# Optimization experiments

Measured on AMD Instinct MI355X. Metric: run time of the kernel, lower is better.

## Reference

```python
import jax, jax.numpy as jnp
import numpy as np

B, D_IN, LAT, C = 16384, 512, 64, 8
HID = [1024, 512, 256]

def _lin(k, fi, fo, scale=0.02):
    k1, k2 = jax.random.split(k)
    return jax.random.normal(k1, (fi, fo), jnp.float32) * scale, jax.random.normal(k2, (fo,), jnp.float32) * scale

def _lin_c(k, fi, fo, scale=0.02):
    k1, k2 = jax.random.split(k)
    return jax.random.normal(k1, (C, fi, fo), jnp.float32) * scale, jax.random.normal(k2, (C, fo), jnp.float32) * scale

def setup_inputs() -> dict:
    key = jax.random.key(0)
    ks = jax.random.split(key, 16)
    x = jax.random.normal(ks[0], (B, D_IN), jnp.float32)
    cluster_labels = jax.random.randint(ks[1], (B,), 0, C, jnp.int32)
    eps = jax.random.normal(ks[2], (B, LAT), jnp.float32)
    # encoder: shared(512->1024), unshared(1024->512), shared(512->256)
    enc_W0, enc_b0 = _lin(ks[3], D_IN, HID[0])
    enc_Wu, enc_bu = _lin_c(ks[4], HID[0], HID[1])
    enc_W2, enc_b2 = _lin(ks[5], HID[1], HID[2])
    # shared latent heads
    mu_W, mu_b = _lin(ks[6], HID[2], LAT)
    lv_W, lv_b = _lin(ks[7], HID[2], LAT)
    # decoder (hidden_dims reversed = [256,512,1024]): unshared(64->256), shared(256->512), unshared(512->1024)
    dec_Wu0, dec_bu0 = _lin_c(ks[8], LAT, HID[2])
    dec_W1, dec_b1 = _lin(ks[9], HID[2], HID[1])
    dec_Wu2, dec_bu2 = _lin_c(ks[10], HID[1], HID[0])
    # per-cluster final layer (1024 -> input_dim), no activation (all-continuous)
    fin_W, fin_b = _lin_c(ks[11], HID[0], D_IN)
    return dict(x=x, cluster_labels=cluster_labels, eps=eps,
                enc_W0=enc_W0, enc_b0=enc_b0, enc_Wu=enc_Wu, enc_bu=enc_bu,
                enc_W2=enc_W2, enc_b2=enc_b2, mu_W=mu_W, mu_b=mu_b,
                lv_W=lv_W, lv_b=lv_b, dec_Wu0=dec_Wu0, dec_bu0=dec_bu0,
                dec_W1=dec_W1, dec_b1=dec_b1, dec_Wu2=dec_Wu2, dec_bu2=dec_bu2,
                fin_W=fin_W, fin_b=fin_b)

def _unshared(h, W, b, labels):
    # per-cluster GEMM then row-wise combine (mask-based dispatch, no row reorder)
    y = jnp.einsum('bi,cio->bco', h, W) + b[None]  # [B, C, out]
    return jnp.take_along_axis(y, labels[:, None, None], axis=1)[:, 0, :]

def reference(x, cluster_labels, eps,
              enc_W0, enc_b0, enc_Wu, enc_bu, enc_W2, enc_b2,
              mu_W, mu_b, lv_W, lv_b,
              dec_Wu0, dec_bu0, dec_W1, dec_b1, dec_Wu2, dec_bu2,
              fin_W, fin_b):
    lbl = cluster_labels.astype(jnp.int32)
    # encoder
    h = jax.nn.relu(x @ enc_W0 + enc_b0)
    h = jax.nn.relu(_unshared(h, enc_Wu, enc_bu, lbl))
    h = jax.nn.relu(h @ enc_W2 + enc_b2)
    mu = h @ mu_W + mu_b
    logvar = h @ lv_W + lv_b
    # reparameterize
    z = mu + jnp.exp(0.5 * logvar) * eps
    # decoder
    h = jax.nn.relu(_unshared(z, dec_Wu0, dec_bu0, lbl))
    h = jax.nn.relu(h @ dec_W1 + dec_b1)
    h = jax.nn.relu(_unshared(h, dec_Wu2, dec_bu2, lbl))
    # per-cluster final output layer (identity activation: all-continuous)
    recon = _unshared(h, fin_W, fin_b, lbl)
    return recon
```

## Files before the change

kernel.cpp:

```cpp
#include <hip/hip_runtime.h>

typedef _Float16 f16;
typedef __attribute__((ext_vector_type(8))) _Float16 f16x8;
typedef __attribute__((ext_vector_type(4))) _Float16 f16x4;
typedef __attribute__((ext_vector_type(4))) float    f32x4;

#define B_ROWS 16384
#define MPAD   17408
#define MTILES 136
#define NBLK   64

typedef __attribute__((address_space(1))) void as1_void;
typedef __attribute__((address_space(3))) void as3_void;

__device__ __forceinline__ void gl_lds16(const void* g, void* l) {
    __builtin_amdgcn_global_load_lds((const as1_void*)g, (as3_void*)l, 16, 0, 0);
}


__global__ __launch_bounds__(256) void k_prep(const int* __restrict__ lbl, int* __restrict__ blockhist,
                                              int* __restrict__ rowmap,
                                              const float* __restrict__ mb_, const float* __restrict__ lb_,
                                              float* __restrict__ bz, f16* __restrict__ zerob) {
    int b = blockIdx.x, t = threadIdx.x;
    int i = b * 256 + t;
    rowmap[i] = -1;
    if (b < NBLK) {
        __shared__ int h[8];
        if (t < 8) h[t] = 0;
        __syncthreads();
        atomicAdd(&h[lbl[i]], 1);
        __syncthreads();
        if (t < 8) blockhist[b * 8 + t] = h[t];
    } else if (b == NBLK) {
        if (t < 64) zerob[t] = (f16)0.f;
        if (t < 64) bz[t] = mb_[t];
        else if (t < 128) bz[t] = lb_[t - 64];
    }
}

__global__ void k_offsets(const int* __restrict__ blockhist, int* offs, int* tilec, int* blockbase) {
    __shared__ int tot[8];
    __shared__ int so[9];
    int t = threadIdx.x;
    if (t < 8) {
        int s = 0;
        for (int b = 0; b < NBLK; ++b) s += blockhist[b * 8 + t];
        tot[t] = s;
    }
    __syncthreads();
    if (t == 0) {
        int o = 0;
        for (int c = 0; c < 8; ++c) { so[c] = o; o += (tot[c] + 127) & ~127; }
        so[8] = o;
        for (int c = 0; c < 9; ++c) offs[c] = so[c];
    }
    __syncthreads();
    if (t < 8) {
        int run = so[t];
        for (int b = 0; b < NBLK; ++b) {
            blockbase[b * 8 + t] = run;
            run += blockhist[b * 8 + t];
        }
    }
    if (t < MTILES) {
        int row = t * 128, c = 7;
        for (int cc = 0; cc < 8; ++cc)
            if (row >= so[cc] && row < so[cc + 1]) c = cc;
        tilec[t] = c;
    }
}

__global__ __launch_bounds__(256) void k_scatter(const int* __restrict__ lbl,
                                                 const int* __restrict__ blockbase,
                                                 int* __restrict__ rowmap) {
    __shared__ int cur[8];
    if (threadIdx.x < 8) cur[threadIdx.x] = blockbase[blockIdx.x * 8 + threadIdx.x];
    __syncthreads();
    int i = blockIdx.x * 256 + threadIdx.x;
    int c = lbl[i];
    int pos = atomicAdd(&cur[c], 1);
    rowmap[pos] = i;
}


struct Seg { const float* s; f16* d; int K, N, b0, nx, ny; long sCS, dCS; };
struct SegTab { Seg g[10]; };

__global__ __launch_bounds__(256) void k_trans(SegTab tab, const float* __restrict__ x, f16* __restrict__ xh) {
    int bid = blockIdx.x;
    int t = threadIdx.x;
    if (bid < tab.g[1].b0) {
        size_t i = (size_t)bid * 256 + t;
        float4 a = ((const float4*)x)[2 * i];
        float4 b = ((const float4*)x)[2 * i + 1];
        f16x8 o = {(f16)a.x, (f16)a.y, (f16)a.z, (f16)a.w,
                   (f16)b.x, (f16)b.y, (f16)b.z, (f16)b.w};
        ((f16x8*)xh)[i] = o;
        return;
    }
    int s = 9;
    while (bid < tab.g[s].b0) --s;
    Seg sg = tab.g[s];
    int lb = bid - sg.b0;
    int nxy = sg.nx * sg.ny;
    int z = lb / nxy; int r = lb - z * nxy;
    int by = r / sg.nx; int bx = r - by * sg.nx;
    const float* src = sg.s + (size_t)z * sg.sCS;
    f16* dst = sg.d + (size_t)z * sg.dCS;
    int n0 = bx * 64, k0 = by * 64;
    __shared__ float ld[64][64];
    int cr = t >> 4, cc = (t & 15) * 4;
    #pragma unroll
    for (int i = 0; i < 4; ++i) {
        float4 v = *(const float4*)(src + (size_t)(k0 + cr + 16 * i) * sg.N + n0 + cc);
        *(float4*)&ld[cr + 16 * i][cc] = v;
    }
    __syncthreads();
    int n = t & 63, gp = t >> 6;
    #pragma unroll
    for (int p = 0; p < 2; ++p) {
        int g = gp + 4 * p;
        f16x8 o;
        #pragma unroll
        for (int j = 0; j < 8; ++j) o[j] = (f16)ld[g * 8 + j][n];
        *(f16x8*)(dst + (size_t)(n0 + n) * sg.K + k0 + g * 8) = o;
    }
}


template<int GATHER, int PERW, int RELU, int EPI>
__global__ __launch_bounds__(256) void gemm_k(
    const f16* __restrict__ A, const f16* __restrict__ Wt,
    const float* __restrict__ bias, f16* __restrict__ Out, float* __restrict__ OutF,
    const float* __restrict__ eps,
    const int* __restrict__ rowmap, const int* __restrict__ tilec,
    const f16* __restrict__ zerobuf, int K, int N)
{
    __shared__ __align__(16) char smem[32768];
    const int tid  = threadIdx.x;
    const int wave = tid >> 6;
    const int lane = tid & 63;

    const int id  = blockIdx.x;
    const int xcd = id & 7;
    const int jj  = id >> 3;
    const int tm  = (jj % 17) * 8 + xcd;
    const int tn  = jj / 17;
    const int r0 = tm * 128, n0 = tn * 128;

    const f16* wb = Wt;
    const float* bb = bias;
    if (PERW) {
        int c = tilec[tm];
        wb += (size_t)c * K * N;
        bb += (size_t)c * N;
    }

    const int srow = tid >> 2;
    const int sg   = tid & 3;
    const int xk16 = (sg ^ ((srow >> 1) & 3)) * 16;
    const size_t rowB = (size_t)K * 2;

    const char* pa[2]; size_t stepA[2];
    #pragma unroll
    for (int p = 0; p < 2; ++p) {
        int gr = r0 + p * 64 + srow;
        if (GATHER) {
            int g = rowmap[gr];
            if (g >= 0) { pa[p] = (const char*)(A + (size_t)g * K) + xk16; stepA[p] = 64; }
            else        { pa[p] = (const char*)zerobuf;                    stepA[p] = 0;  }
        } else {
            pa[p] = (const char*)(A + (size_t)gr * K) + xk16; stepA[p] = 64;
        }
    }
    const char* pb = (const char*)(wb + (size_t)(n0 + srow) * K) + xk16;
    const size_t pbOff = 64 * rowB;

    const int mb = (wave >> 1) * 64;
    const int nb = (wave & 1) * 64;
    const int quad = lane >> 4;
    const int r16  = lane & 15;
    const int off  = (quad ^ ((r16 >> 1) & 3)) * 16;

    float bv[4];
    #pragma unroll
    for (int j = 0; j < 4; ++j) bv[j] = bb[n0 + nb + j * 16 + r16];

    f32x4 acc[4][4];
    #pragma unroll
    for (int i = 0; i < 4; ++i)
        #pragma unroll
        for (int j = 0; j < 4; ++j)
            acc[i][j] = (f32x4){0.f, 0.f, 0.f, 0.f};

    auto stage = [&](char* dst) {
        gl_lds16(pa[0], dst        + wave * 1024);
        gl_lds16(pa[1], dst + 4096 + wave * 1024);
        gl_lds16(pb,           dst + 8192  + wave * 1024);
        gl_lds16(pb + pbOff,   dst + 12288 + wave * 1024);
        pa[0] += stepA[0]; pa[1] += stepA[1];
        pb += 64;
    };

    auto compute = [&](const char* base) {
        const char* lA = base;
        const char* lB = base + 8192;
        f16x8 af[4], bf[4];
        #pragma unroll
        for (int i = 0; i < 4; ++i)
            af[i] = *(const f16x8*)(lA + (mb + i * 16 + r16) * 64 + off);
        #pragma unroll
        for (int j = 0; j < 4; ++j)
            bf[j] = *(const f16x8*)(lB + (nb + j * 16 + r16) * 64 + off);
        #pragma unroll
        for (int i = 0; i < 4; ++i)
            #pragma unroll
            for (int j = 0; j < 4; ++j)
                acc[i][j] = __builtin_amdgcn_mfma_f32_16x16x32_f16(af[i], bf[j], acc[i][j], 0, 0, 0);
    };

    const int nk = K >> 5;
    stage(smem);
    __syncthreads();
    int cur = 0;
    for (int kb = 0; kb < nk - 1; ++kb) {
        stage(smem + ((cur ^ 1) << 14));
        compute(smem + (cur << 14));
        __syncthreads();
        cur ^= 1;
    }
    compute(smem + (cur << 14));

    if (EPI == 2) {
        __syncthreads();
        #pragma unroll
        for (int i = 0; i < 4; ++i) {
            #pragma unroll
            for (int r = 0; r < 4; ++r) {
                int lr = mb + i * 16 + quad * 4 + r;
                #pragma unroll
                for (int j = 0; j < 4; ++j) {
                    int lc = nb + j * 16 + r16;
                    float v = acc[i][j][r] + bv[j];
                    *(f16*)(smem + lr * 256 + ((((lc >> 3) ^ (lr & 7))) << 4) + ((lc & 7) << 1)) = (f16)v;
                }
            }
        }
        __syncthreads();
        const int col = tid & 63;
        const int rb  = tid >> 6;
        for (int rr = 0; rr < 32; ++rr) {
            int row = rb * 32 + rr;
            int g = rowmap[r0 + row];
            float e = (g >= 0) ? eps[(size_t)g * 64 + col] : 0.f;
            float mu = (float)*(const f16*)(smem + row * 256 + ((((col >> 3) ^ (row & 7))) << 4) + ((col & 7) << 1));
            int c2 = col + 64;
            float lv = (float)*(const f16*)(smem + row * 256 + ((((c2 >> 3) ^ (row & 7))) << 4) + ((c2 & 7) << 1));
            Out[(size_t)(r0 + row) * 64 + col] = (f16)(mu + expf(0.5f * lv) * e);
        }
        return;
    }

    #pragma unroll
    for (int i = 0; i < 4; ++i) {
        #pragma unroll
        for (int r = 0; r < 4; ++r) {
            int orow = r0 + mb + i * 16 + quad * 4 + r;
            int g = 0;
            if (EPI == 1) g = rowmap[orow];
            #pragma unroll
            for (int j = 0; j < 4; ++j) {
                int ocol = n0 + nb + j * 16 + r16;
                float v = acc[i][j][r] + bv[j];
                if (RELU) v = fmaxf(v, 0.f);
                if (EPI == 1) {
                    if (g >= 0) OutF[(size_t)g * N + ocol] = v;
                } else {
                    Out[(size_t)orow * N + ocol] = (f16)v;
                }
            }
        }
    }
}


extern "C" void kernel_launch(void* const* d_in, const int* in_sizes, int n_in,
                              void* d_out, int out_size, void* d_ws, size_t ws_size,
                              hipStream_t stream) {
    const float* x      = (const float*)d_in[0];
    const int*   lbl    = (const int*)  d_in[1];
    const float* eps    = (const float*)d_in[2];
    const float* enc_W0 = (const float*)d_in[3];
    const float* enc_b0 = (const float*)d_in[4];
    const float* enc_Wu = (const float*)d_in[5];
    const float* enc_bu = (const float*)d_in[6];
    const float* enc_W2 = (const float*)d_in[7];
    const float* enc_b2 = (const float*)d_in[8];
    const float* mu_W   = (const float*)d_in[9];
    const float* mu_b   = (const float*)d_in[10];
    const float* lv_W   = (const float*)d_in[11];
    const float* lv_b   = (const float*)d_in[12];
    const float* dWu0   = (const float*)d_in[13];
    const float* dbu0   = (const float*)d_in[14];
    const float* dW1    = (const float*)d_in[15];
    const float* db1    = (const float*)d_in[16];
    const float* dWu2   = (const float*)d_in[17];
    const float* dbu2   = (const float*)d_in[18];
    const float* finW   = (const float*)d_in[19];
    const float* finb   = (const float*)d_in[20];
    float* out = (float*)d_out;
    (void)in_sizes; (void)n_in; (void)out_size; (void)ws_size;

    char* base = (char*)d_ws;
    size_t off = 0;
    auto alloc = [&](size_t bytes) { char* r = base + off; off = (off + bytes + 255) & ~(size_t)255; return r; };
    f16* xh     = (f16*)alloc((size_t)B_ROWS * 512 * 2);
    f16* buf1   = (f16*)alloc((size_t)MPAD * 1024 * 2);
    f16* buf2   = (f16*)alloc((size_t)MPAD * 512 * 2);
    f16* buf3   = (f16*)alloc((size_t)MPAD * 256 * 2);
    f16* zb     = (f16*)alloc((size_t)MPAD * 64 * 2);
    f16* w0t    = (f16*)alloc(1024ul * 512 * 2);
    f16* wut    = (f16*)alloc(8ul * 512 * 1024 * 2);
    f16* w2t    = (f16*)alloc(256ul * 512 * 2);
    f16* wzt    = (f16*)alloc(128ul * 256 * 2);
    f16* wd0t   = (f16*)alloc(8ul * 256 * 64 * 2);
    f16* wd1t   = (f16*)alloc(512ul * 256 * 2);
    f16* wd2t   = (f16*)alloc(8ul * 1024 * 512 * 2);
    f16* wft    = (f16*)alloc(8ul * 512 * 1024 * 2);
    float* bz   = (float*)alloc(128 * 4);
    int* rowmap = (int*)alloc(MPAD * 4);
    int* blockhist = (int*)alloc(NBLK * 8 * 4);
    int* blockbase = (int*)alloc(NBLK * 8 * 4);
    int* offs   = (int*)alloc(64);
    int* tilec  = (int*)alloc(MTILES * 4);
    f16* zerob  = (f16*)alloc(256);

    k_prep<<<MPAD / 256, 256, 0, stream>>>(lbl, blockhist, rowmap, mu_b, lv_b, bz, zerob);
    k_offsets<<<1, 256, 0, stream>>>(blockhist, offs, tilec, blockbase);
    k_scatter<<<NBLK, 256, 0, stream>>>(lbl, blockbase, rowmap);

    SegTab tab;
    int b0 = B_ROWS * 512 / 8 / 256;
    auto seg = [&](int i, const float* s, f16* d, int K, int N, int nz, long sCS, long dCS) {
        int nx = N / 64, ny = K / 64;
        tab.g[i] = Seg{s, d, K, N, b0, nx, ny, sCS, dCS};
        b0 += nx * ny * nz;
    };
    tab.g[0] = Seg{nullptr, nullptr, 0, 0, 0, 0, 0, 0, 0};
    seg(1, enc_W0, w0t, 512, 1024, 1, 0, 0);
    seg(2, enc_Wu, wut, 1024, 512, 8, 1024l * 512, 512l * 1024);
    seg(3, enc_W2, w2t, 512, 256, 1, 0, 0);
    seg(4, mu_W, wzt, 256, 64, 1, 0, 0);
    seg(5, lv_W, wzt + 64 * 256, 256, 64, 1, 0, 0);
    seg(6, dWu0, wd0t, 64, 256, 8, 64l * 256, 256l * 64);
    seg(7, dW1, wd1t, 256, 512, 1, 0, 0);
    seg(8, dWu2, wd2t, 512, 1024, 8, 512l * 1024, 1024l * 512);
    seg(9, finW, wft, 1024, 512, 8, 1024l * 512, 512l * 1024);
    k_trans<<<b0, 256, 0, stream>>>(tab, x, xh);

    gemm_k<1,0,1,0><<<MTILES * 8, 256, 0, stream>>>(xh,   w0t,  enc_b0, buf1, nullptr, nullptr, rowmap, tilec, zerob, 512, 1024);
    gemm_k<0,1,1,0><<<MTILES * 4, 256, 0, stream>>>(buf1, wut,  enc_bu, buf2, nullptr, nullptr, rowmap, tilec, zerob, 1024, 512);
    gemm_k<0,0,1,0><<<MTILES * 2, 256, 0, stream>>>(buf2, w2t,  enc_b2, buf3, nullptr, nullptr, rowmap, tilec, zerob, 512, 256);
    gemm_k<0,0,0,2><<<MTILES * 1, 256, 0, stream>>>(buf3, wzt,  bz,     zb,   nullptr, eps,     rowmap, tilec, zerob, 256, 128);
    gemm_k<0,1,1,0><<<MTILES * 2, 256, 0, stream>>>(zb,   wd0t, dbu0,   buf3, nullptr, nullptr, rowmap, tilec, zerob, 64, 256);
    gemm_k<0,0,1,0><<<MTILES * 4, 256, 0, stream>>>(buf3, wd1t, db1,    buf2, nullptr, nullptr, rowmap, tilec, zerob, 256, 512);
    gemm_k<0,1,1,0><<<MTILES * 8, 256, 0, stream>>>(buf2, wd2t, dbu2,   buf1, nullptr, nullptr, rowmap, tilec, zerob, 512, 1024);
    gemm_k<0,1,0,1><<<MTILES * 4, 256, 0, stream>>>(buf1, wft,  finb,   nullptr, out,  nullptr, rowmap, tilec, zerob, 1024, 512);
}
```

Baseline: 363.2 us.

## Fuse all prep, transpose and GEMM launches into one persistent kernel with grid barriers

Replaces about a dozen kernel launches with a single persistent kernel that walks virtual tiles in phases, separated by atomic grid-wide barriers. Weight transposes are spread across phases so they overlap with earlier GEMMs. The change also swizzles the transpose's shared-memory layout, switches the GEMM main loop to explicit vmcnt waits plus raw s_barrier, and uses nontemporal stores. It removes launch gaps and tail idle time, but it depends on every block being co-resident for the spin barriers, and its runtime-flag GEMM loses the template specialisation.

```diff
diff --git a/kernel.cpp b/kernel.cpp
--- a/kernel.cpp
+++ b/kernel.cpp
@@ -2,7 +2,6 @@
 
 typedef _Float16 f16;
 typedef __attribute__((ext_vector_type(8))) _Float16 f16x8;
-typedef __attribute__((ext_vector_type(4))) _Float16 f16x4;
 typedef __attribute__((ext_vector_type(4))) float    f32x4;
 
 #define B_ROWS 16384
@@ -16,17 +15,44 @@
 __device__ __forceinline__ void gl_lds16(const void* g, void* l) {
     __builtin_amdgcn_global_load_lds((const as1_void*)g, (as3_void*)l, 16, 0, 0);
 }
-
-
-__global__ __launch_bounds__(256) void k_prep(const int* __restrict__ lbl, int* __restrict__ blockhist,
-                                              int* __restrict__ rowmap,
-                                              const float* __restrict__ mb_, const float* __restrict__ lb_,
-                                              float* __restrict__ bz, f16* __restrict__ zerob) {
-    int b = blockIdx.x, t = threadIdx.x;
+template<typename T>
+__device__ __forceinline__ void st_nt(T* p, T v) { __builtin_nontemporal_store(v, p); }
+
+struct Seg   { const float* s; f16* d; int K, N, nx, ny; long sCS, dCS; };
+struct GemmL { const f16* A; const f16* Wt; const float* bias; f16* OutH; float* OutF; int K, N, flags; };
+
+struct Mega {
+    Seg   sg[10];
+    GemmL L[8];
+    const float* x; f16* xh;
+    const int* lbl; const float* mb; const float* lb; float* bz; f16* zerob;
+    int* blockhist; int* blockbase; int* offs; int* tilec; int* rowmap;
+    const float* eps; int* done;
+};
+
+__device__ __forceinline__ void phase_barrier(int p, int* done) {
+    __syncthreads();
+    if (threadIdx.x == 0) {
+        __threadfence();
+        __hip_atomic_fetch_add(&done[p], 1, __ATOMIC_RELEASE, __HIP_MEMORY_SCOPE_AGENT);
+        while (__hip_atomic_load(&done[p], __ATOMIC_RELAXED, __HIP_MEMORY_SCOPE_AGENT) < (int)gridDim.x)
+            __builtin_amdgcn_s_sleep(8);
+    }
+    __syncthreads();
+    __threadfence();
+}
+
+
+__device__ __forceinline__ void prep_body(char* smemraw, int b, const int* __restrict__ lbl,
+        int* __restrict__ blockhist, int* __restrict__ rowmap,
+        const float* __restrict__ mb_, const float* __restrict__ lb_,
+        float* __restrict__ bz, f16* __restrict__ zerob) {
+    int* h = (int*)smemraw;
+    int t = threadIdx.x;
     int i = b * 256 + t;
     rowmap[i] = -1;
     if (b < NBLK) {
-        __shared__ int h[8];
+        __syncthreads();
         if (t < 8) h[t] = 0;
         __syncthreads();
         atomicAdd(&h[lbl[i]], 1);
@@ -39,10 +65,12 @@
     }
 }
 
-__global__ void k_offsets(const int* __restrict__ blockhist, int* offs, int* tilec, int* blockbase) {
-    __shared__ int tot[8];
-    __shared__ int so[9];
+__device__ __forceinline__ void offsets_body(char* smemraw, const int* __restrict__ blockhist,
+        int* __restrict__ offs, int* __restrict__ tilec, int* __restrict__ blockbase) {
+    int* tot = (int*)smemraw;
+    int* so  = tot + 8;
     int t = threadIdx.x;
+    __syncthreads();
     if (t < 8) {
         int s = 0;
         for (int b = 0; b < NBLK; ++b) s += blockhist[b * 8 + t];
@@ -71,94 +99,68 @@
     }
 }
 
-__global__ __launch_bounds__(256) void k_scatter(const int* __restrict__ lbl,
-                                                 const int* __restrict__ blockbase,
-                                                 int* __restrict__ rowmap) {
-    __shared__ int cur[8];
-    if (threadIdx.x < 8) cur[threadIdx.x] = blockbase[blockIdx.x * 8 + threadIdx.x];
-    __syncthreads();
-    int i = blockIdx.x * 256 + threadIdx.x;
+__device__ __forceinline__ void scatter_body(char* smemraw, int b, const int* __restrict__ lbl,
+        const int* __restrict__ blockbase, int* __restrict__ rowmap) {
+    int* cur = (int*)smemraw;
+    __syncthreads();
+    if (threadIdx.x < 8) cur[threadIdx.x] = blockbase[b * 8 + threadIdx.x];
+    __syncthreads();
+    int i = b * 256 + threadIdx.x;
     int c = lbl[i];
     int pos = atomicAdd(&cur[c], 1);
     rowmap[pos] = i;
 }
 
-
-struct Seg { const float* s; f16* d; int K, N, b0, nx, ny; long sCS, dCS; };
-struct SegTab { Seg g[10]; };
-
-__global__ __launch_bounds__(256) void k_trans(SegTab tab, const float* __restrict__ x, f16* __restrict__ xh) {
-    int bid = blockIdx.x;
+__device__ __forceinline__ void trans_tile(char* smemraw, Seg sg, int lb) {
+    float (*ld)[64] = (float(*)[64])smemraw;
     int t = threadIdx.x;
-    if (bid < tab.g[1].b0) {
-        size_t i = (size_t)bid * 256 + t;
-        float4 a = ((const float4*)x)[2 * i];
-        float4 b = ((const float4*)x)[2 * i + 1];
-        f16x8 o = {(f16)a.x, (f16)a.y, (f16)a.z, (f16)a.w,
-                   (f16)b.x, (f16)b.y, (f16)b.z, (f16)b.w};
-        ((f16x8*)xh)[i] = o;
-        return;
-    }
-    int s = 9;
-    while (bid < tab.g[s].b0) --s;
-    Seg sg = tab.g[s];
-    int lb = bid - sg.b0;
     int nxy = sg.nx * sg.ny;
     int z = lb / nxy; int r = lb - z * nxy;
     int by = r / sg.nx; int bx = r - by * sg.nx;
     const float* src = sg.s + (size_t)z * sg.sCS;
     f16* dst = sg.d + (size_t)z * sg.dCS;
     int n0 = bx * 64, k0 = by * 64;
-    __shared__ float ld[64][64];
     int cr = t >> 4, cc = (t & 15) * 4;
+    __syncthreads();
     #pragma unroll
     for (int i = 0; i < 4; ++i) {
-        float4 v = *(const float4*)(src + (size_t)(k0 + cr + 16 * i) * sg.N + n0 + cc);
-        *(float4*)&ld[cr + 16 * i][cc] = v;
-    }
-    __syncthreads();
-    int n = t & 63, gp = t >> 6;
+        int rr = cr + 16 * i;
+        float4 v = *(const float4*)(src + (size_t)(k0 + rr) * sg.N + n0 + cc);
+        *(float4*)&ld[rr][(((cc >> 2) ^ (rr & 15)) << 2)] = v;
+    }
+    __syncthreads();
     #pragma unroll
     for (int p = 0; p < 2; ++p) {
-        int g = gp + 4 * p;
+        int G = p * 256 + t;
+        int n = G >> 3, gg = G & 7;
         f16x8 o;
         #pragma unroll
-        for (int j = 0; j < 8; ++j) o[j] = (f16)ld[g * 8 + j][n];
-        *(f16x8*)(dst + (size_t)(n0 + n) * sg.K + k0 + g * 8) = o;
-    }
-}
-
-
-template<int GATHER, int PERW, int RELU, int EPI>
-__global__ __launch_bounds__(256) void gemm_k(
-    const f16* __restrict__ A, const f16* __restrict__ Wt,
-    const float* __restrict__ bias, f16* __restrict__ Out, float* __restrict__ OutF,
-    const float* __restrict__ eps,
-    const int* __restrict__ rowmap, const int* __restrict__ tilec,
-    const f16* __restrict__ zerobuf, int K, int N)
+        for (int j = 0; j < 8; ++j) {
+            int kk = gg * 8 + j;
+            o[j] = (f16)ld[kk][(((n >> 2) ^ (kk & 15)) << 2) | (n & 3)];
+        }
+        *(f16x8*)(dst + (size_t)(n0 + n) * sg.K + k0 + gg * 8) = o;
+    }
+}
+
+__device__ __forceinline__ void gemm_tile(char* smem, int vt, GemmL L,
+        const int* __restrict__ rowmap, const int* __restrict__ tilec,
+        const f16* __restrict__ zerobuf, const float* __restrict__ eps)
 {
-    __shared__ __align__(16) char smem[32768];
     const int tid  = threadIdx.x;
     const int wave = tid >> 6;
     const int lane = tid & 63;
-
-    const int id  = blockIdx.x;
-    const int xcd = id & 7;
-    const int jj  = id >> 3;
-    const int tm  = (jj % 17) * 8 + xcd;
-    const int tn  = jj / 17;
+    const int xcd = vt & 7, jj = vt >> 3;
+    const int tm = (jj % 17) * 8 + xcd;
+    const int tn = jj / 17;
     const int r0 = tm * 128, n0 = tn * 128;
-
-    const f16* wb = Wt;
-    const float* bb = bias;
-    if (PERW) {
-        int c = tilec[tm];
-        wb += (size_t)c * K * N;
-        bb += (size_t)c * N;
-    }
-
-    const int srow = tid >> 2;
-    const int sg   = tid & 3;
+    const int K = L.K, N = L.N;
+
+    const f16* wb = L.Wt;
+    const float* bb = L.bias;
+    if (L.flags & 2) { int c = tilec[tm]; wb += (size_t)c * K * N; bb += (size_t)c * N; }
+
+    const int srow = tid >> 2, sg = tid & 3;
     const int xk16 = (sg ^ ((srow >> 1) & 3)) * 16;
     const size_t rowB = (size_t)K * 2;
 
@@ -166,21 +168,19 @@
     #pragma unroll
     for (int p = 0; p < 2; ++p) {
         int gr = r0 + p * 64 + srow;
-        if (GATHER) {
+        if (L.flags & 1) {
             int g = rowmap[gr];
-            if (g >= 0) { pa[p] = (const char*)(A + (size_t)g * K) + xk16; stepA[p] = 64; }
-            else        { pa[p] = (const char*)zerobuf;                    stepA[p] = 0;  }
+            if (g >= 0) { pa[p] = (const char*)(L.A + (size_t)g * K) + xk16; stepA[p] = 64; }
+            else        { pa[p] = (const char*)zerobuf;                      stepA[p] = 0;  }
         } else {
-            pa[p] = (const char*)(A + (size_t)gr * K) + xk16; stepA[p] = 64;
+            pa[p] = (const char*)(L.A + (size_t)gr * K) + xk16; stepA[p] = 64;
         }
     }
     const char* pb = (const char*)(wb + (size_t)(n0 + srow) * K) + xk16;
     const size_t pbOff = 64 * rowB;
 
-    const int mb = (wave >> 1) * 64;
-    const int nb = (wave & 1) * 64;
-    const int quad = lane >> 4;
-    const int r16  = lane & 15;
+    const int mb = (wave >> 1) * 64, nb = (wave & 1) * 64;
+    const int quad = lane >> 4, r16 = lane & 15;
     const int off  = (quad ^ ((r16 >> 1) & 3)) * 16;
 
     float bv[4];
@@ -195,14 +195,13 @@
             acc[i][j] = (f32x4){0.f, 0.f, 0.f, 0.f};
 
     auto stage = [&](char* dst) {
-        gl_lds16(pa[0], dst        + wave * 1024);
-        gl_lds16(pa[1], dst + 4096 + wave * 1024);
+        gl_lds16(pa[0],        dst         + wave * 1024);
+        gl_lds16(pa[1],        dst + 4096  + wave * 1024);
         gl_lds16(pb,           dst + 8192  + wave * 1024);
         gl_lds16(pb + pbOff,   dst + 12288 + wave * 1024);
         pa[0] += stepA[0]; pa[1] += stepA[1];
         pb += 64;
     };
-
     auto compute = [&](const char* base) {
         const char* lA = base;
         const char* lB = base + 8192;
@@ -220,19 +219,24 @@
                 acc[i][j] = __builtin_amdgcn_mfma_f32_16x16x32_f16(af[i], bf[j], acc[i][j], 0, 0, 0);
     };
 
+    __syncthreads();
+
     const int nk = K >> 5;
     stage(smem);
-    __syncthreads();
     int cur = 0;
     for (int kb = 0; kb < nk - 1; ++kb) {
         stage(smem + ((cur ^ 1) << 14));
+        asm volatile("s_waitcnt vmcnt(4)" ::: "memory");
+        __builtin_amdgcn_s_barrier();
         compute(smem + (cur << 14));
-        __syncthreads();
+        __builtin_amdgcn_s_barrier();
         cur ^= 1;
     }
+    asm volatile("s_waitcnt vmcnt(0)" ::: "memory");
+    __builtin_amdgcn_s_barrier();
     compute(smem + (cur << 14));
 
-    if (EPI == 2) {
+    if (L.flags & 16) {
         __syncthreads();
         #pragma unroll
         for (int i = 0; i < 4; ++i) {
@@ -257,7 +261,7 @@
             float mu = (float)*(const f16*)(smem + row * 256 + ((((col >> 3) ^ (row & 7))) << 4) + ((col & 7) << 1));
             int c2 = col + 64;
             float lv = (float)*(const f16*)(smem + row * 256 + ((((c2 >> 3) ^ (row & 7))) << 4) + ((c2 & 7) << 1));
-            Out[(size_t)(r0 + row) * 64 + col] = (f16)(mu + expf(0.5f * lv) * e);
+            st_nt(&L.OutH[(size_t)(r0 + row) * 64 + col], (f16)(mu + expf(0.5f * lv) * e));
         }
         return;
     }
@@ -268,20 +272,84 @@
         for (int r = 0; r < 4; ++r) {
             int orow = r0 + mb + i * 16 + quad * 4 + r;
             int g = 0;
-            if (EPI == 1) g = rowmap[orow];
+            if (L.flags & 8) g = rowmap[orow];
             #pragma unroll
             for (int j = 0; j < 4; ++j) {
                 int ocol = n0 + nb + j * 16 + r16;
                 float v = acc[i][j][r] + bv[j];
-                if (RELU) v = fmaxf(v, 0.f);
-                if (EPI == 1) {
-                    if (g >= 0) OutF[(size_t)g * N + ocol] = v;
+                if (L.flags & 4) v = fmaxf(v, 0.f);
+                if (L.flags & 8) {
+                    if (g >= 0) st_nt(&L.OutF[(size_t)g * N + ocol], v);
                 } else {
-                    Out[(size_t)orow * N + ocol] = (f16)v;
+                    st_nt(&L.OutH[(size_t)orow * N + ocol], (f16)v);
                 }
             }
         }
     }
+}
+
+
+__global__ __launch_bounds__(256) void k_zero(int* done) {
+    if (threadIdx.x < 16) done[threadIdx.x] = 0;
+}
+
+__global__ __launch_bounds__(256) void megak(Mega M) {
+    __shared__ __align__(16) char smem[32768];
+    const int bid = blockIdx.x;
+    const int t = threadIdx.x;
+    const int G = gridDim.x;
+
+    for (int vt = bid; vt < 68 + 4096 + 128; vt += G) {
+        if (vt < 68) {
+            prep_body(smem, vt, M.lbl, M.blockhist, M.rowmap, M.mb, M.lb, M.bz, M.zerob);
+        } else if (vt < 68 + 4096) {
+            size_t i = (size_t)(vt - 68) * 256 + t;
+            float4 a = ((const float4*)M.x)[2 * i];
+            float4 b = ((const float4*)M.x)[2 * i + 1];
+            f16x8 o = {(f16)a.x, (f16)a.y, (f16)a.z, (f16)a.w,
+                       (f16)b.x, (f16)b.y, (f16)b.z, (f16)b.w};
+            st_nt(&((f16x8*)M.xh)[i], o);
+        } else {
+            trans_tile(smem, M.sg[1], vt - (68 + 4096));
+        }
+    }
+    phase_barrier(0, M.done);
+
+    for (int vt = bid; vt < 105; vt += G) {
+        if (vt == 0)       offsets_body(smem, M.blockhist, M.offs, M.tilec, M.blockbase);
+        else if (vt < 33)  trans_tile(smem, M.sg[3], vt - 1);
+        else if (vt < 37)  trans_tile(smem, M.sg[4], vt - 33);
+        else if (vt < 41)  trans_tile(smem, M.sg[5], vt - 37);
+        else if (vt < 73)  trans_tile(smem, M.sg[6], vt - 41);
+        else               trans_tile(smem, M.sg[7], vt - 73);
+    }
+    phase_barrier(1, M.done);
+
+    for (int vt = bid; vt < 64; vt += G)
+        scatter_body(smem, vt, M.lbl, M.blockbase, M.rowmap);
+    phase_barrier(2, M.done);
+
+    for (int vt = bid; vt < 1024 + 1088 + 1024 + 1024; vt += G) {
+        if (vt < 1024)       trans_tile(smem, M.sg[2], vt);
+        else if (vt < 2112)  gemm_tile(smem, vt - 1024, M.L[0], M.rowmap, M.tilec, M.zerob, M.eps);
+        else if (vt < 3136)  trans_tile(smem, M.sg[8], vt - 2112);
+        else                 trans_tile(smem, M.sg[9], vt - 3136);
+    }
+    phase_barrier(3, M.done);
+
+    for (int vt = bid; vt < 544; vt += G)  gemm_tile(smem, vt, M.L[1], M.rowmap, M.tilec, M.zerob, M.eps);
+    phase_barrier(4, M.done);
+    for (int vt = bid; vt < 272; vt += G)  gemm_tile(smem, vt, M.L[2], M.rowmap, M.tilec, M.zerob, M.eps);
+    phase_barrier(5, M.done);
+    for (int vt = bid; vt < 136; vt += G)  gemm_tile(smem, vt, M.L[3], M.rowmap, M.tilec, M.zerob, M.eps);
+    phase_barrier(6, M.done);
+    for (int vt = bid; vt < 272; vt += G)  gemm_tile(smem, vt, M.L[4], M.rowmap, M.tilec, M.zerob, M.eps);
+    phase_barrier(7, M.done);
+    for (int vt = bid; vt < 544; vt += G)  gemm_tile(smem, vt, M.L[5], M.rowmap, M.tilec, M.zerob, M.eps);
+    phase_barrier(8, M.done);
+    for (int vt = bid; vt < 1088; vt += G) gemm_tile(smem, vt, M.L[6], M.rowmap, M.tilec, M.zerob, M.eps);
+    phase_barrier(9, M.done);
+    for (int vt = bid; vt < 544; vt += G)  gemm_tile(smem, vt, M.L[7], M.rowmap, M.tilec, M.zerob, M.eps);
 }
 
 
@@ -335,36 +403,39 @@
     int* offs   = (int*)alloc(64);
     int* tilec  = (int*)alloc(MTILES * 4);
     f16* zerob  = (f16*)alloc(256);
-
-    k_prep<<<MPAD / 256, 256, 0, stream>>>(lbl, blockhist, rowmap, mu_b, lv_b, bz, zerob);
-    k_offsets<<<1, 256, 0, stream>>>(blockhist, offs, tilec, blockbase);
-    k_scatter<<<NBLK, 256, 0, stream>>>(lbl, blockbase, rowmap);
-
-    SegTab tab;
-    int b0 = B_ROWS * 512 / 8 / 256;
-    auto seg = [&](int i, const float* s, f16* d, int K, int N, int nz, long sCS, long dCS) {
-        int nx = N / 64, ny = K / 64;
-        tab.g[i] = Seg{s, d, K, N, b0, nx, ny, sCS, dCS};
-        b0 += nx * ny * nz;
-    };
-    tab.g[0] = Seg{nullptr, nullptr, 0, 0, 0, 0, 0, 0, 0};
-    seg(1, enc_W0, w0t, 512, 1024, 1, 0, 0);
-    seg(2, enc_Wu, wut, 1024, 512, 8, 1024l * 512, 512l * 1024);
-    seg(3, enc_W2, w2t, 512, 256, 1, 0, 0);
-    seg(4, mu_W, wzt, 256, 64, 1, 0, 0);
-    seg(5, lv_W, wzt + 64 * 256, 256, 64, 1, 0, 0);
-    seg(6, dWu0, wd0t, 64, 256, 8, 64l * 256, 256l * 64);
-    seg(7, dW1, wd1t, 256, 512, 1, 0, 0);
-    seg(8, dWu2, wd2t, 512, 1024, 8, 512l * 1024, 1024l * 512);
-    seg(9, finW, wft, 1024, 512, 8, 1024l * 512, 512l * 1024);
-    k_trans<<<b0, 256, 0, stream>>>(tab, x, xh);
-
-    gemm_k<1,0,1,0><<<MTILES * 8, 256, 0, stream>>>(xh,   w0t,  enc_b0, buf1, nullptr, nullptr, rowmap, tilec, zerob, 512, 1024);
-    gemm_k<0,1,1,0><<<MTILES * 4, 256, 0, stream>>>(buf1, wut,  enc_bu, buf2, nullptr, nullptr, rowmap, tilec, zerob, 1024, 512);
-    gemm_k<0,0,1,0><<<MTILES * 2, 256, 0, stream>>>(buf2, w2t,  enc_b2, buf3, nullptr, nullptr, rowmap, tilec, zerob, 512, 256);
-    gemm_k<0,0,0,2><<<MTILES * 1, 256, 0, stream>>>(buf3, wzt,  bz,     zb,   nullptr, eps,     rowmap, tilec, zerob, 256, 128);
-    gemm_k<0,1,1,0><<<MTILES * 2, 256, 0, stream>>>(zb,   wd0t, dbu0,   buf3, nullptr, nullptr, rowmap, tilec, zerob, 64, 256);
-    gemm_k<0,0,1,0><<<MTILES * 4, 256, 0, stream>>>(buf3, wd1t, db1,    buf2, nullptr, nullptr, rowmap, tilec, zerob, 256, 512);
-    gemm_k<0,1,1,0><<<MTILES * 8, 256, 0, stream>>>(buf2, wd2t, dbu2,   buf1, nullptr, nullptr, rowmap, tilec, zerob, 512, 1024);
-    gemm_k<0,1,0,1><<<MTILES * 4, 256, 0, stream>>>(buf1, wft,  finb,   nullptr, out,  nullptr, rowmap, tilec, zerob, 1024, 512);
-}
+    int* done   = (int*)alloc(64);
+
+    Mega M;
+    M.sg[1] = Seg{enc_W0, w0t, 512, 1024, 16, 8, 0, 0};
+    M.sg[2] = Seg{enc_Wu, wut, 1024, 512, 8, 16, 1024l * 512, 512l * 1024};
+    M.sg[3] = Seg{enc_W2, w2t, 512, 256, 4, 8, 0, 0};
+    M.sg[4] = Seg{mu_W, wzt, 256, 64, 1, 4, 0, 0};
+    M.sg[5] = Seg{lv_W, wzt + 64 * 256, 256, 64, 1, 4, 0, 0};
+    M.sg[6] = Seg{dWu0, wd0t, 64, 256, 4, 1, 64l * 256, 256l * 64};
+    M.sg[7] = Seg{dW1, wd1t, 256, 512, 8, 4, 0, 0};
+    M.sg[8] = Seg{dWu2, wd2t, 512, 1024, 16, 8, 512l * 1024, 1024l * 512};
+    M.sg[9] = Seg{finW, wft, 1024, 512, 8, 16, 1024l * 512, 512l * 1024};
+    M.sg[0] = Seg{nullptr, nullptr, 0, 0, 0, 0, 0, 0};
+    M.L[0] = GemmL{xh,   w0t,  enc_b0, buf1, nullptr, 512, 1024, 1 | 4};
+    M.L[1] = GemmL{buf1, wut,  enc_bu, buf2, nullptr, 1024, 512, 2 | 4};
+    M.L[2] = GemmL{buf2, w2t,  enc_b2, buf3, nullptr, 512, 256, 4};
+    M.L[3] = GemmL{buf3, wzt,  bz,     zb,   nullptr, 256, 128, 16};
+    M.L[4] = GemmL{zb,   wd0t, dbu0,   buf3, nullptr, 64, 256, 2 | 4};
+    M.L[5] = GemmL{buf3, wd1t, db1,    buf2, nullptr, 256, 512, 4};
+    M.L[6] = GemmL{buf2, wd2t, dbu2,   buf1, nullptr, 512, 1024, 2 | 4};
+    M.L[7] = GemmL{buf1, wft,  finb,   nullptr, out,  1024, 512, 2 | 8};
+    M.x = x; M.xh = xh;
+    M.lbl = lbl; M.mb = mu_b; M.lb = lv_b; M.bz = bz; M.zerob = zerob;
+    M.blockhist = blockhist; M.blockbase = blockbase; M.offs = offs;
+    M.tilec = tilec; M.rowmap = rowmap;
+    M.eps = eps; M.done = done;
+
+    int maxb = 0;
+    if (hipOccupancyMaxActiveBlocksPerMultiprocessor(&maxb, megak, 256, 0) != hipSuccess || maxb < 1)
+        maxb = 1;
+    int grid = maxb * 256;
+    if (grid > 512) grid = 512;
+
+    k_zero<<<1, 64, 0, stream>>>(done);
+    megak<<<grid, 256, 0, stream>>>(M);
+}
```

After: 998.5 us. 175% more time.
